# Kernel tuning notes

Measured on AMD Instinct MI355X. Metric: run time of the kernel, lower is better.

## Reference

```python
import jax, jax.numpy as jnp
import numpy as np

# 0-indexed channel groups (fixed constants from the source)
_G1 = np.array([2, 1, 3, 4, 5, 7, 8, 9, 10, 11, 12, 13]) - 1
_G2 = np.array([6, 14, 15, 16, 22, 23, 24, 25, 31, 32, 33, 34, 40, 41, 42, 43, 49, 50]) - 1
_G3 = np.array([17, 18, 19, 20, 21, 26, 27, 28, 29, 30, 35, 36, 37, 38, 39, 44, 45, 46, 47, 48]) - 1
_G4 = np.array([51, 52, 53, 54, 55, 56, 57, 58, 59, 60, 61, 62]) - 1
_GROUPS = [_G1, _G2, _G3, _G4]

B, DIM, NCLS = 2048, 512, 62
_CHN = [12, 18, 20, 12]


def setup_inputs() -> dict:
    key = jax.random.key(0)
    ks = jax.random.split(key, 20)
    inp = {}
    for i, ch in enumerate(_CHN):
        inp[f"x_{i+1}"] = jax.random.normal(ks[i], (B, ch, DIM), dtype=jnp.float32)
    inp["g"] = jax.random.normal(ks[4], (B, NCLS, DIM), dtype=jnp.float32)
    for i in range(4):
        inp[f"logits_{i+1}"] = jax.random.normal(ks[5 + i], (B, NCLS), dtype=jnp.float32)
    for i, ch in enumerate(_CHN):
        fan_in = DIM * ch
        bound = 1.0 / np.sqrt(fan_in)
        inp[f"W{i+1}"] = jax.random.uniform(ks[9 + 2 * i], (fan_in, 1), minval=-bound, maxval=bound, dtype=jnp.float32)
        inp[f"b{i+1}"] = jax.random.uniform(ks[10 + 2 * i], (1,), minval=-bound, maxval=bound, dtype=jnp.float32)
    return inp


def _confidence(logits):
    # confidence = max_prob * (1 - normalized_entropy), shape [B, 1]
    p = jax.nn.softmax(logits, axis=1)
    max_p = p.max(axis=1)
    ent = -jnp.sum(p * jnp.log(p + 1e-8), axis=1)
    norm_ent = ent / jnp.log(jnp.float32(logits.shape[1]))
    return (max_p * (1.0 - norm_ent))[:, None]


def reference(x_1, x_2, x_3, x_4, g, logits_1, logits_2, logits_3, logits_4,
              W1, b1, W2, b2, W3, b3, W4, b4):
    Bsz = x_1.shape[0]
    confs = jnp.concatenate([_confidence(l) for l in (logits_1, logits_2, logits_3, logits_4)], axis=1)  # [B,4]
    norm_conf = jax.nn.softmax(confs, axis=1)
    xs = (x_1, x_2, x_3, x_4)
    Ws = (W1, W2, W3, W4)
    bs = (b1, b2, b3, b4)
    trans = jnp.zeros_like(g)
    for i in range(4):
        u = jax.nn.sigmoid(xs[i].reshape(Bsz, -1) @ Ws[i] + bs[i])  # [B,1]
        u_final = u * norm_conf[:, i:i + 1]                          # [B,1]
        x_region = g[:, _GROUPS[i], :]                               # gather [B,ch,dim]
        x_total = (xs[i] + x_region) * u_final[:, :, None]
        trans = trans.at[:, _GROUPS[i], :].set(x_total)              # scatter (index_copy)
    return (norm_conf[:, 0:1], norm_conf[:, 1:2], norm_conf[:, 2:3], norm_conf[:, 3:4], trans)
```

## Files before the change

### kernel.cpp

```cpp
#include <hip/hip_runtime.h>
#include <math.h>

#define BATCH 2048
#define NCLS 62

__device__ __forceinline__ float wave_max(float v) {
#pragma unroll
    for (int m = 32; m >= 1; m >>= 1) v = fmaxf(v, __shfl_xor(v, m, 64));
    return v;
}
__device__ __forceinline__ float wave_sum(float v) {
#pragma unroll
    for (int m = 32; m >= 1; m >>= 1) v += __shfl_xor(v, m, 64);
    return v;
}

__global__ __launch_bounds__(256) void head_kernel(
    const float* __restrict__ x1, const float* __restrict__ x2,
    const float* __restrict__ x3, const float* __restrict__ x4,
    const float* __restrict__ lg1, const float* __restrict__ lg2,
    const float* __restrict__ lg3, const float* __restrict__ lg4,
    const float* __restrict__ W1, const float* __restrict__ bb1,
    const float* __restrict__ W2, const float* __restrict__ bb2,
    const float* __restrict__ W3, const float* __restrict__ bb3,
    const float* __restrict__ W4, const float* __restrict__ bb4,
    float* __restrict__ out_nc, float* __restrict__ s_out)
{
    const int b    = blockIdx.x;
    const int tid  = threadIdx.x;
    const int wave = tid >> 6;
    const int lane = tid & 63;

    __shared__ float conf_s[4];
    __shared__ float part_s[4][4];

    {
        const float* lg = (wave == 0) ? lg1 : (wave == 1) ? lg2 : (wave == 2) ? lg3 : lg4;
        float v = (lane < NCLS) ? lg[b * NCLS + lane] : -INFINITY;
        float m = wave_max(v);
        float e = (lane < NCLS) ? __expf(v - m) : 0.0f;
        float S = wave_sum(e);
        float p = e / S;
        float t = (lane < NCLS) ? p * __logf(p + 1e-8f) : 0.0f;
        float ent = -wave_sum(t);
        float conf = (1.0f / S) * (1.0f - ent * 0.242298797f);
        if (lane == 0) conf_s[wave] = conf;
    }
    __syncthreads();

    const int fan4[4] = {1536, 2304, 2560, 1536};
    const float4* xv[4] = {(const float4*)x1, (const float4*)x2,
                           (const float4*)x3, (const float4*)x4};
    const float4* wv[4] = {(const float4*)W1, (const float4*)W2,
                           (const float4*)W3, (const float4*)W4};
#pragma unroll
    for (int i = 0; i < 4; ++i) {
        const float4* xp = xv[i] + (size_t)b * fan4[i];
        const float4* wp = wv[i];
        float a = 0.0f;
        for (int j = tid; j < fan4[i]; j += 256) {
            float4 xx = xp[j];
            float4 ww = wp[j];
            a += xx.x * ww.x + xx.y * ww.y + xx.z * ww.z + xx.w * ww.w;
        }
        a = wave_sum(a);
        if (lane == 0) part_s[wave][i] = a;
    }
    __syncthreads();

    if (tid < 4) {
        const int i = tid;
        float dot = part_s[0][i] + part_s[1][i] + part_s[2][i] + part_s[3][i];
        float bias = (i == 0) ? bb1[0] : (i == 1) ? bb2[0] : (i == 2) ? bb3[0] : bb4[0];
        float u = 1.0f / (1.0f + __expf(-(dot + bias)));
        float c0 = conf_s[0], c1 = conf_s[1], c2 = conf_s[2], c3 = conf_s[3];
        float m4 = fmaxf(fmaxf(c0, c1), fmaxf(c2, c3));
        float e0 = __expf(c0 - m4), e1 = __expf(c1 - m4);
        float e2 = __expf(c2 - m4), e3 = __expf(c3 - m4);
        float S4 = e0 + e1 + e2 + e3;
        float ei = (i == 0) ? e0 : (i == 1) ? e1 : (i == 2) ? e2 : e3;
        float nc = ei / S4;
        out_nc[i * BATCH + b] = nc;
        s_out[b * 4 + i] = u * nc;
    }
}

__device__ const unsigned char GRP_TBL[62] = {
    0,0,0,0,0, 1, 0,0,0,0,0,0,0,
    1,1,1,
    2,2,2,2,2,
    1,1,1,1,
    2,2,2,2,2,
    1,1,1,1,
    2,2,2,2,2,
    1,1,1,1,
    2,2,2,2,2,
    1,1,
    3,3,3,3,3,3,3,3,3,3,3,3
};
__device__ const unsigned char CHAN_TBL[62] = {
    1,0,2,3,4, 0, 5,6,7,8,9,10,11,
    1,2,3,
    0,1,2,3,4,
    4,5,6,7,
    5,6,7,8,9,
    8,9,10,11,
    10,11,12,13,14,
    12,13,14,15,
    15,16,17,18,19,
    16,17,
    0,1,2,3,4,5,6,7,8,9,10,11
};

__global__ __launch_bounds__(256) void trans_kernel(
    const float4* __restrict__ x1, const float4* __restrict__ x2,
    const float4* __restrict__ x3, const float4* __restrict__ x4,
    const float4* __restrict__ g, const float* __restrict__ s,
    float4* __restrict__ out)
{
    int idx = blockIdx.x * 256 + threadIdx.x;
    int d4  = idx & 127;
    int row = idx >> 7;
    int b   = row / 62;
    int r   = row - b * 62;
    int grp = GRP_TBL[r];
    int ch  = CHAN_TBL[r];
    const float4* xp;
    int chN;
    if (grp == 0)      { xp = x1; chN = 12; }
    else if (grp == 1) { xp = x2; chN = 18; }
    else if (grp == 2) { xp = x3; chN = 20; }
    else               { xp = x4; chN = 12; }
    float sc = s[b * 4 + grp];
    float4 xx = xp[((size_t)b * chN + ch) * 128 + d4];
    float4 gg = g[(size_t)row * 128 + d4];
    float4 o;
    o.x = (xx.x + gg.x) * sc;
    o.y = (xx.y + gg.y) * sc;
    o.z = (xx.z + gg.z) * sc;
    o.w = (xx.w + gg.w) * sc;
    out[(size_t)row * 128 + d4] = o;
}

extern "C" void kernel_launch(void* const* d_in, const int* in_sizes, int n_in,
                              void* d_out, int out_size, void* d_ws, size_t ws_size,
                              hipStream_t stream) {
    const float* x1  = (const float*)d_in[0];
    const float* x2  = (const float*)d_in[1];
    const float* x3  = (const float*)d_in[2];
    const float* x4  = (const float*)d_in[3];
    const float* g   = (const float*)d_in[4];
    const float* lg1 = (const float*)d_in[5];
    const float* lg2 = (const float*)d_in[6];
    const float* lg3 = (const float*)d_in[7];
    const float* lg4 = (const float*)d_in[8];
    const float* W1  = (const float*)d_in[9];
    const float* b1  = (const float*)d_in[10];
    const float* W2  = (const float*)d_in[11];
    const float* b2  = (const float*)d_in[12];
    const float* W3  = (const float*)d_in[13];
    const float* b3  = (const float*)d_in[14];
    const float* W4  = (const float*)d_in[15];
    const float* b4  = (const float*)d_in[16];

    float* out  = (float*)d_out;
    float* s_ws = (float*)d_ws;

    head_kernel<<<BATCH, 256, 0, stream>>>(
        x1, x2, x3, x4, lg1, lg2, lg3, lg4,
        W1, b1, W2, b2, W3, b3, W4, b4,
        out, s_ws);

    int total_f4 = BATCH * 62 * 128;
    trans_kernel<<<total_f4 / 256, 256, 0, stream>>>(
        (const float4*)x1, (const float4*)x2, (const float4*)x3, (const float4*)x4,
        (const float4*)g, s_ws, (float4*)(out + 4 * BATCH));
}
```

Before: 642.1 us.

## Fuse head and trans kernels, staging x in LDS for reuse

Merges the confidence/gating head and the gather-scatter output into one kernel with one 512-thread block per batch row. Each block loads its x slices once into shared memory while computing the dot products. It then reuses them from LDS for the output pass, instead of re-reading x from global memory in a second kernel. The cost is about 127KB of static LDS per block, which allows only one block per CU and lowers latency hiding. The load phase and the streaming phase also run serially within each block.

```diff
diff --git a/kernel.cpp b/kernel.cpp
--- a/kernel.cpp
+++ b/kernel.cpp
@@ -3,6 +3,7 @@
 
 #define BATCH 2048
 #define NCLS 62
+#define TPB 512
 
 __device__ __forceinline__ float wave_max(float v) {
 #pragma unroll
@@ -13,76 +14,6 @@
 #pragma unroll
     for (int m = 32; m >= 1; m >>= 1) v += __shfl_xor(v, m, 64);
     return v;
-}
-
-__global__ __launch_bounds__(256) void head_kernel(
-    const float* __restrict__ x1, const float* __restrict__ x2,
-    const float* __restrict__ x3, const float* __restrict__ x4,
-    const float* __restrict__ lg1, const float* __restrict__ lg2,
-    const float* __restrict__ lg3, const float* __restrict__ lg4,
-    const float* __restrict__ W1, const float* __restrict__ bb1,
-    const float* __restrict__ W2, const float* __restrict__ bb2,
-    const float* __restrict__ W3, const float* __restrict__ bb3,
-    const float* __restrict__ W4, const float* __restrict__ bb4,
-    float* __restrict__ out_nc, float* __restrict__ s_out)
-{
-    const int b    = blockIdx.x;
-    const int tid  = threadIdx.x;
-    const int wave = tid >> 6;
-    const int lane = tid & 63;
-
-    __shared__ float conf_s[4];
-    __shared__ float part_s[4][4];
-
-    {
-        const float* lg = (wave == 0) ? lg1 : (wave == 1) ? lg2 : (wave == 2) ? lg3 : lg4;
-        float v = (lane < NCLS) ? lg[b * NCLS + lane] : -INFINITY;
-        float m = wave_max(v);
-        float e = (lane < NCLS) ? __expf(v - m) : 0.0f;
-        float S = wave_sum(e);
-        float p = e / S;
-        float t = (lane < NCLS) ? p * __logf(p + 1e-8f) : 0.0f;
-        float ent = -wave_sum(t);
-        float conf = (1.0f / S) * (1.0f - ent * 0.242298797f);
-        if (lane == 0) conf_s[wave] = conf;
-    }
-    __syncthreads();
-
-    const int fan4[4] = {1536, 2304, 2560, 1536};
-    const float4* xv[4] = {(const float4*)x1, (const float4*)x2,
-                           (const float4*)x3, (const float4*)x4};
-    const float4* wv[4] = {(const float4*)W1, (const float4*)W2,
-                           (const float4*)W3, (const float4*)W4};
-#pragma unroll
-    for (int i = 0; i < 4; ++i) {
-        const float4* xp = xv[i] + (size_t)b * fan4[i];
-        const float4* wp = wv[i];
-        float a = 0.0f;
-        for (int j = tid; j < fan4[i]; j += 256) {
-            float4 xx = xp[j];
-            float4 ww = wp[j];
-            a += xx.x * ww.x + xx.y * ww.y + xx.z * ww.z + xx.w * ww.w;
-        }
-        a = wave_sum(a);
-        if (lane == 0) part_s[wave][i] = a;
-    }
-    __syncthreads();
-
-    if (tid < 4) {
-        const int i = tid;
-        float dot = part_s[0][i] + part_s[1][i] + part_s[2][i] + part_s[3][i];
-        float bias = (i == 0) ? bb1[0] : (i == 1) ? bb2[0] : (i == 2) ? bb3[0] : bb4[0];
-        float u = 1.0f / (1.0f + __expf(-(dot + bias)));
-        float c0 = conf_s[0], c1 = conf_s[1], c2 = conf_s[2], c3 = conf_s[3];
-        float m4 = fmaxf(fmaxf(c0, c1), fmaxf(c2, c3));
-        float e0 = __expf(c0 - m4), e1 = __expf(c1 - m4);
-        float e2 = __expf(c2 - m4), e3 = __expf(c3 - m4);
-        float S4 = e0 + e1 + e2 + e3;
-        float ei = (i == 0) ? e0 : (i == 1) ? e1 : (i == 2) ? e2 : e3;
-        float nc = ei / S4;
-        out_nc[i * BATCH + b] = nc;
-        s_out[b * 4 + i] = u * nc;
-    }
 }
 
 __device__ const unsigned char GRP_TBL[62] = {
@@ -112,34 +43,116 @@
     0,1,2,3,4,5,6,7,8,9,10,11
 };
 
-__global__ __launch_bounds__(256) void trans_kernel(
+__global__ __launch_bounds__(TPB) void fused_kernel(
     const float4* __restrict__ x1, const float4* __restrict__ x2,
     const float4* __restrict__ x3, const float4* __restrict__ x4,
-    const float4* __restrict__ g, const float* __restrict__ s,
-    float4* __restrict__ out)
+    const float4* __restrict__ g,
+    const float* __restrict__ lg1, const float* __restrict__ lg2,
+    const float* __restrict__ lg3, const float* __restrict__ lg4,
+    const float4* __restrict__ W1, const float* __restrict__ bb1,
+    const float4* __restrict__ W2, const float* __restrict__ bb2,
+    const float4* __restrict__ W3, const float* __restrict__ bb3,
+    const float4* __restrict__ W4, const float* __restrict__ bb4,
+    float* __restrict__ out_nc, float4* __restrict__ out_trans)
 {
-    int idx = blockIdx.x * 256 + threadIdx.x;
-    int d4  = idx & 127;
-    int row = idx >> 7;
-    int b   = row / 62;
-    int r   = row - b * 62;
-    int grp = GRP_TBL[r];
-    int ch  = CHAN_TBL[r];
-    const float4* xp;
-    int chN;
-    if (grp == 0)      { xp = x1; chN = 12; }
-    else if (grp == 1) { xp = x2; chN = 18; }
-    else if (grp == 2) { xp = x3; chN = 20; }
-    else               { xp = x4; chN = 12; }
-    float sc = s[b * 4 + grp];
-    float4 xx = xp[((size_t)b * chN + ch) * 128 + d4];
-    float4 gg = g[(size_t)row * 128 + d4];
-    float4 o;
-    o.x = (xx.x + gg.x) * sc;
-    o.y = (xx.y + gg.y) * sc;
-    o.z = (xx.z + gg.z) * sc;
-    o.w = (xx.w + gg.w) * sc;
-    out[(size_t)row * 128 + d4] = o;
+    __shared__ float4 x_s[7936];
+    __shared__ float conf_s[4];
+    __shared__ float part_s[8][4];
+    __shared__ float s_s[4];
+
+    const int b    = blockIdx.x;
+    const int tid  = threadIdx.x;
+    const int wave = tid >> 6;
+    const int lane = tid & 63;
+
+    const int fan4[4]  = {1536, 2304, 2560, 1536};
+    const int base4[4] = {0, 1536, 3840, 6400};
+    const float4* xv[4] = {x1, x2, x3, x4};
+    const float4* wv[4] = {W1, W2, W3, W4};
+
+    float acc0 = 0.f, acc1 = 0.f, acc2 = 0.f, acc3 = 0.f;
+#pragma unroll
+    for (int i = 0; i < 4; ++i) {
+        const float4* xp = xv[i] + (size_t)b * fan4[i];
+        const float4* wp = wv[i];
+        float a = 0.f;
+#pragma unroll 4
+        for (int j = tid; j < fan4[i]; j += TPB) {
+            float4 xx = xp[j];
+            float4 ww = wp[j];
+            x_s[base4[i] + j] = xx;
+            a += xx.x * ww.x + xx.y * ww.y + xx.z * ww.z + xx.w * ww.w;
+        }
+        if (i == 0) acc0 = a; else if (i == 1) acc1 = a;
+        else if (i == 2) acc2 = a; else acc3 = a;
+    }
+    {
+        float a0 = wave_sum(acc0);
+        float a1 = wave_sum(acc1);
+        float a2 = wave_sum(acc2);
+        float a3 = wave_sum(acc3);
+        if (lane == 0) {
+            part_s[wave][0] = a0; part_s[wave][1] = a1;
+            part_s[wave][2] = a2; part_s[wave][3] = a3;
+        }
+    }
+
+    if (wave < 4) {
+        const float* lg = (wave == 0) ? lg1 : (wave == 1) ? lg2
+                        : (wave == 2) ? lg3 : lg4;
+        float v = (lane < NCLS) ? lg[b * NCLS + lane] : -INFINITY;
+        float m = wave_max(v);
+        float e = (lane < NCLS) ? __expf(v - m) : 0.0f;
+        float S = wave_sum(e);
+        float p = e / S;
+        float t = (lane < NCLS) ? p * __logf(p + 1e-8f) : 0.0f;
+        float ent = -wave_sum(t);
+        float conf = (1.0f / S) * (1.0f - ent * 0.242298797f);
+        if (lane == 0) conf_s[wave] = conf;
+    }
+    __syncthreads();
+
+    if (tid < 4) {
+        const int i = tid;
+        float dot = 0.f;
+#pragma unroll
+        for (int w = 0; w < 8; ++w) dot += part_s[w][i];
+        float bias = (i == 0) ? bb1[0] : (i == 1) ? bb2[0]
+                   : (i == 2) ? bb3[0] : bb4[0];
+        float u = 1.0f / (1.0f + __expf(-(dot + bias)));
+        float c0 = conf_s[0], c1 = conf_s[1], c2 = conf_s[2], c3 = conf_s[3];
+        float m4 = fmaxf(fmaxf(c0, c1), fmaxf(c2, c3));
+        float e0 = __expf(c0 - m4), e1 = __expf(c1 - m4);
+        float e2 = __expf(c2 - m4), e3 = __expf(c3 - m4);
+        float S4 = e0 + e1 + e2 + e3;
+        float ei = (i == 0) ? e0 : (i == 1) ? e1 : (i == 2) ? e2 : e3;
+        float nc = ei / S4;
+        out_nc[i * BATCH + b] = nc;
+        s_s[i] = u * nc;
+    }
+    __syncthreads();
+
+    const float4* gp = g + (size_t)b * 7936;
+    float4*       op = out_trans + (size_t)b * 7936;
+#pragma unroll 4
+    for (int k = 0; k < 16; ++k) {
+        int idx = tid + k * TPB;
+        if (idx < 7936) {
+            int row = idx >> 7;
+            int d4  = idx & 127;
+            int grp = GRP_TBL[row];
+            int ch  = CHAN_TBL[row];
+            float sc = s_s[grp];
+            float4 xx = x_s[base4[grp] + ch * 128 + d4];
+            float4 gg = gp[idx];
+            float4 o;
+            o.x = (xx.x + gg.x) * sc;
+            o.y = (xx.y + gg.y) * sc;
+            o.z = (xx.z + gg.z) * sc;
+            o.w = (xx.w + gg.w) * sc;
+            op[idx] = o;
+        }
+    }
 }
 
 extern "C" void kernel_launch(void* const* d_in, const int* in_sizes, int n_in,
@@ -163,16 +176,14 @@
     const float* W4  = (const float*)d_in[15];
     const float* b4  = (const float*)d_in[16];
 
-    float* out  = (float*)d_out;
-    float* s_ws = (float*)d_ws;
+    float* out = (float*)d_out;
+    float4* out_trans = (float4*)(out + 4 * BATCH);
 
-    head_kernel<<<BATCH, 256, 0, stream>>>(
-        x1, x2, x3, x4, lg1, lg2, lg3, lg4,
-        W1, b1, W2, b2, W3, b3, W4, b4,
-        out, s_ws);
-
-    int total_f4 = BATCH * 62 * 128;
-    trans_kernel<<<total_f4 / 256, 256, 0, stream>>>(
+    fused_kernel<<<BATCH, TPB, 0, stream>>>(
         (const float4*)x1, (const float4*)x2, (const float4*)x3, (const float4*)x4,
-        (const float4*)g, s_ws, (float4*)(out + 4 * BATCH));
+        (const float4*)g,
+        lg1, lg2, lg3, lg4,
+        (const float4*)W1, b1, (const float4*)W2, b2,
+        (const float4*)W3, b3, (const float4*)W4, b4,
+        out, out_trans);
 }
```

After: 648.4 us. About the same (+1.0%).
